# Kernel tuning notes

Hardware: AMD Instinct MI355X
Metric: run time of the kernel (lower is better)

The kernel has to match this reference:

```python
import jax, jax.numpy as jnp
import numpy as np

D = 1024        # inputsize / d_model
G = 8           # groupnum (KV groups)
H = 16          # heads per group
DQ = 128        # qk head dim
DV = 128        # v head dim
FF = 1024       # ffoutsize
B, S = 1, 1024


def _rmsnorm(t, gamma, d_model):
    # torch F.normalize(x, dim=-1) * sqrt(d_model) * gamma
    n = jnp.sqrt(jnp.sum(t * t, axis=-1, keepdims=True))
    return t / jnp.maximum(n, 1e-12) * (d_model ** 0.5) * gamma


def setup_inputs() -> dict:
    key = jax.random.key(0)
    ks = jax.random.split(key, 8)
    std = 0.02
    x = jax.random.normal(ks[0], (B, S, D), dtype=jnp.float32)
    gamma_in = jnp.ones((D,), jnp.float32)
    Wq_w = jax.random.normal(ks[1], (H * G * DQ, D), jnp.float32) * std
    Wq_b = jnp.zeros((H * G * DQ,), jnp.float32)
    Wkv_w = jax.random.normal(ks[2], (G * (DQ + DV), D), jnp.float32) * std
    Wkv_b = jnp.zeros((G * (DQ + DV),), jnp.float32)
    gamma_z = jnp.ones((G * H * DV,), jnp.float32)
    W1 = jax.random.normal(ks[3], (FF * 2, G * H * DV), jnp.float32) * std
    b1 = jnp.zeros((FF * 2,), jnp.float32)
    W2 = jax.random.normal(ks[4], (FF, FF * 2), jnp.float32) * std
    b2 = jnp.zeros((FF,), jnp.float32)
    return {"x": x, "gamma_in": gamma_in, "Wq_w": Wq_w, "Wq_b": Wq_b,
            "Wkv_w": Wkv_w, "Wkv_b": Wkv_b, "gamma_z": gamma_z,
            "W1": W1, "b1": b1, "W2": W2, "b2": b2}


def reference(x, gamma_in, Wq_w, Wq_b, Wkv_w, Wkv_b, gamma_z, W1, b1, W2, b2):
    x = _rmsnorm(x, gamma_in, D)                      # (B,S,D)
    # self-attention path (m is None -> m = x)
    q = (x @ Wq_w.T + Wq_b).reshape(B, S, G, H, DQ)   # (B,S,G,H,dq)
    kv = x @ Wkv_w.T + Wkv_b                          # (B,S,G*(dq+dv))
    k, v = jnp.split(kv, 2, axis=-1)
    k = k.reshape(B, S, G, DQ)                        # (B,S,G,dq)
    v = v.reshape(B, S, G, DV)                        # (B,S,G,dv)
    scale = 1.0 / (DQ ** 0.5)
    scores = jnp.einsum('bsghd,bTgd->bghsT', q, k) * scale  # (B,G,H,S,S)
    attn = jax.nn.softmax(scores, axis=-1)
    z = jnp.einsum('bghsT,bTgd->bsghd', attn, v)      # (B,S,G,H,dv)
    z = z.reshape(B, S, G * H * DV)
    z = _rmsnorm(z, gamma_z, G * H * DV)
    h1 = jax.nn.silu(z @ W1.T + b1)                   # (B,S,2*FF)
    out = jax.nn.silu(h1 @ W2.T + b2)                 # (B,S,FF)
    return out
```

## Files before the change

kernel.cpp:

```cpp
#include <hip/hip_runtime.h>
#include <hip/hip_bf16.h>
#include <math.h>

typedef __attribute__((ext_vector_type(8))) short short8;
typedef __attribute__((ext_vector_type(4))) float floatx4;

__device__ __forceinline__ ushort f2bf(float f) {
  __hip_bfloat16 h = __float2bfloat16(f);
  return *reinterpret_cast<ushort*>(&h);
}
__device__ __forceinline__ float bf2f(ushort u) {
  union { unsigned int i; float f; } c; c.i = ((unsigned)u) << 16; return c.f;
}

__device__ __forceinline__ void lds_dma16(const void* g, void* l) {
  __builtin_amdgcn_global_load_lds((const __attribute__((address_space(1))) void*)g,
                                   (__attribute__((address_space(3))) void*)l, 16, 0, 0);
}

__global__ __launch_bounds__(256) void cvt_all(const float* __restrict__ p0, ushort* __restrict__ o0, int b0,
                                               const float* __restrict__ p1, ushort* __restrict__ o1, int b1,
                                               const float* __restrict__ p2, ushort* __restrict__ o2, int b2,
                                               const float* __restrict__ p3, ushort* __restrict__ o3) {
  int b = blockIdx.x;
  const float* in; ushort* out; int base;
  if (b < b0)            { in = p0; out = o0; base = 0; }
  else if (b < b0 + b1)  { in = p1; out = o1; base = b0; }
  else if (b < b0 + b1 + b2) { in = p2; out = o2; base = b0 + b1; }
  else                   { in = p3; out = o3; base = b0 + b1 + b2; }
  int i = (b - base) * 256 + threadIdx.x;
  float4 v = ((const float4*)in)[i];
  ushort4 o;
  o.x = f2bf(v.x); o.y = f2bf(v.y); o.z = f2bf(v.z); o.w = f2bf(v.w);
  ((ushort4*)out)[i] = o;
}

__global__ __launch_bounds__(256) void rmsnorm_f32(const float* __restrict__ x,
                                                   const float* __restrict__ gamma,
                                                   ushort* __restrict__ y, int D, float sqrtD) {
  const int row = blockIdx.x;
  const float* xr = x + (size_t)row * D;
  float ss = 0.f;
  for (int i = threadIdx.x * 4; i < D; i += 1024) {
    float4 v = *(const float4*)&xr[i];
    ss += v.x * v.x + v.y * v.y + v.z * v.z + v.w * v.w;
  }
#pragma unroll
  for (int off = 1; off < 64; off <<= 1) ss += __shfl_xor(ss, off);
  __shared__ float red[4];
  if ((threadIdx.x & 63) == 0) red[threadIdx.x >> 6] = ss;
  __syncthreads();
  ss = red[0] + red[1] + red[2] + red[3];
  const float sc = sqrtD / fmaxf(sqrtf(ss), 1e-12f);
  for (int i = threadIdx.x * 4; i < D; i += 1024) {
    float4 v = *(const float4*)&xr[i];
    ushort4 o;
    o.x = f2bf(v.x * sc * gamma[i]);
    o.y = f2bf(v.y * sc * gamma[i + 1]);
    o.z = f2bf(v.z * sc * gamma[i + 2]);
    o.w = f2bf(v.w * sc * gamma[i + 3]);
    *(ushort4*)&y[(size_t)row * D + i] = o;
  }
}

__global__ __launch_bounds__(256) void rmsnorm_bf16(const ushort* __restrict__ x,
                                                    const float* __restrict__ gamma,
                                                    ushort* __restrict__ y, int D, float sqrtD) {
  const int row = blockIdx.x;
  const ushort* xr = x + (size_t)row * D;
  float ss = 0.f;
  for (int i = threadIdx.x * 8; i < D; i += 2048) {
    short8 v = *(const short8*)&xr[i];
#pragma unroll
    for (int e = 0; e < 8; e++) { float f = bf2f((ushort)v[e]); ss += f * f; }
  }
#pragma unroll
  for (int off = 1; off < 64; off <<= 1) ss += __shfl_xor(ss, off);
  __shared__ float red[4];
  if ((threadIdx.x & 63) == 0) red[threadIdx.x >> 6] = ss;
  __syncthreads();
  ss = red[0] + red[1] + red[2] + red[3];
  const float sc = sqrtD / fmaxf(sqrtf(ss), 1e-12f);
  for (int i = threadIdx.x * 8; i < D; i += 2048) {
    short8 v = *(const short8*)&xr[i];
    short8 ov;
#pragma unroll
    for (int e = 0; e < 8; e++) ov[e] = (short)f2bf(bf2f((ushort)v[e]) * sc * gamma[i + e]);
    *(short8*)&y[(size_t)row * D + i] = ov;
  }
}

template <int EPI, int ACT, int OUTBF16>
__global__ __launch_bounds__(256, 3) void gemm3(const ushort* __restrict__ A,
                                                const ushort* __restrict__ B,
                                                const float* __restrict__ bias,
                                                const float* __restrict__ bias2,
                                                void* __restrict__ C1,
                                                void* __restrict__ C2,
                                                int M, int N, int K, int Ksplit, float scale) {
  __shared__ ushort As[128 * 64];
  __shared__ ushort Bs[128 * 64];
  const int tid = threadIdx.x;
  const int wave = tid >> 6;
  const int lane = tid & 63;
  const int c16 = lane & 15;
  const int quad = lane >> 4;
  const int wm = wave >> 1;
  const int wn = wave & 1;
  const size_t m0 = (size_t)blockIdx.x * 128;
  const size_t n0 = (size_t)blockIdx.y * 128;
  const int kbeg = blockIdx.z * Ksplit;
  const int kend = kbeg + Ksplit;

  const int rsub = lane >> 3;
  const int csw = (lane & 7) ^ rsub;

  const floatx4 zero = {0.f, 0.f, 0.f, 0.f};
  floatx4 acc[4][4];
#pragma unroll
  for (int a = 0; a < 4; a++)
#pragma unroll
    for (int b = 0; b < 4; b++) acc[a][b] = zero;

  for (int k0 = kbeg; k0 < kend; k0 += 64) {
    __syncthreads();
#pragma unroll
    for (int i = 0; i < 4; i++) {
      const int j = wave * 4 + i;
      const int r = j * 8 + rsub;
      lds_dma16(&A[(m0 + r) * K + k0 + csw * 8], (void*)(As + j * 512));
      lds_dma16(&B[(n0 + r) * K + k0 + csw * 8], (void*)(Bs + j * 512));
    }
    __syncthreads();
#pragma unroll
    for (int kc = 0; kc < 2; kc++) {
      short8 af[4], bf4[4];
#pragma unroll
      for (int mt = 0; mt < 4; mt++) {
        const int row = wm * 64 + mt * 16 + c16;
        af[mt] = *(const short8*)&As[row * 64 + (((kc * 4 + quad) ^ (row & 7)) << 3)];
      }
#pragma unroll
      for (int nt = 0; nt < 4; nt++) {
        const int row = wn * 64 + nt * 16 + c16;
        bf4[nt] = *(const short8*)&Bs[row * 64 + (((kc * 4 + quad) ^ (row & 7)) << 3)];
      }
#pragma unroll
      for (int mt = 0; mt < 4; mt++)
#pragma unroll
        for (int nt = 0; nt < 4; nt++)
          acc[mt][nt] = __builtin_amdgcn_mfma_f32_16x16x32_bf16(af[mt], bf4[nt], acc[mt][nt], 0, 0, 0);
    }
  }

#pragma unroll
  for (int mt = 0; mt < 4; mt++) {
#pragma unroll
    for (int nt = 0; nt < 4; nt++) {
      const size_t col = n0 + wn * 64 + nt * 16 + c16;
      const size_t row0 = m0 + wm * 64 + mt * 16 + quad * 4;
      if (EPI == 0) {
        const float bv = bias[col];
#pragma unroll
        for (int r = 0; r < 4; r++) {
          float v = acc[mt][nt][r] + bv;
          if (ACT) v = v / (1.f + __expf(-v));
          if (OUTBF16) ((ushort*)C1)[(row0 + r) * N + col] = f2bf(v);
          else         ((float*)C1)[(row0 + r) * N + col] = v;
        }
      } else if (EPI == 1) {
        float* plane = (float*)C1 + (size_t)blockIdx.z * M * N;
#pragma unroll
        for (int r = 0; r < 4; r++)
          plane[(row0 + r) * N + col] = acc[mt][nt][r];
      } else {
        if (col < 16384) {
          const float bv = bias[col];
#pragma unroll
          for (int r = 0; r < 4; r++)
            ((ushort*)C1)[(row0 + r) * 16384 + col] = f2bf((acc[mt][nt][r] + bv) * scale);
        } else {
          const size_t ckv = col - 16384;
          const float bv = bias2[ckv];
#pragma unroll
          for (int r = 0; r < 4; r++)
            ((ushort*)C2)[(row0 + r) * 2048 + ckv] = f2bf(acc[mt][nt][r] + bv);
        }
      }
    }
  }
}

template <int NZ, int OUTBF16>
__global__ __launch_bounds__(256) void epi_sum_silu(const float* __restrict__ accb,
                                                    const float* __restrict__ bias,
                                                    void* __restrict__ outp, int N, int n4,
                                                    size_t plane4) {
  int i = blockIdx.x * 256 + threadIdx.x;
  if (i >= n4) return;
  float4 v = ((const float4*)accb)[i];
#pragma unroll
  for (int z = 1; z < NZ; z++) {
    float4 p = ((const float4*)accb)[i + z * plane4];
    v.x += p.x; v.y += p.y; v.z += p.z; v.w += p.w;
  }
  const float4 b = *(const float4*)&bias[(i * 4) % N];
  v.x += b.x; v.y += b.y; v.z += b.z; v.w += b.w;
  v.x = v.x / (1.f + __expf(-v.x));
  v.y = v.y / (1.f + __expf(-v.y));
  v.z = v.z / (1.f + __expf(-v.z));
  v.w = v.w / (1.f + __expf(-v.w));
  if (OUTBF16) {
    ushort4 o; o.x = f2bf(v.x); o.y = f2bf(v.y); o.z = f2bf(v.z); o.w = f2bf(v.w);
    ((ushort4*)outp)[i] = o;
  } else {
    ((float4*)outp)[i] = v;
  }
}

__global__ __launch_bounds__(256) void vtrans(const ushort* __restrict__ KV,
                                              ushort* __restrict__ VT) {
  __shared__ ushort Vl[64 * 138];
  const int tid = threadIdx.x;
  const int t0 = blockIdx.x * 64;
  const int g = blockIdx.y;
#pragma unroll
  for (int i = 0; i < 16; i++) {
    int idx = tid + i * 256;
    int r = idx >> 6, dc = idx & 63;
    *(uint*)&Vl[r * 138 + dc * 2] =
        *(const uint*)&KV[(size_t)(t0 + r) * 2048 + 1024 + g * 128 + dc * 2];
  }
  __syncthreads();
#pragma unroll
  for (int i = 0; i < 4; i++) {
    int idx = tid + i * 256;
    int dv = idx >> 3, tch = idx & 7;
    short8 o;
#pragma unroll
    for (int j = 0; j < 8; j++) o[j] = (short)Vl[(tch * 8 + j) * 138 + dv];
    *(short8*)&VT[(size_t)g * 131072 + (size_t)dv * 1024 + t0 + tch * 8] = o;
  }
}

__global__ __launch_bounds__(512, 2) void attn6(const ushort* __restrict__ Q,
                                                const ushort* __restrict__ KV,
                                                const ushort* __restrict__ VT,
                                                ushort* __restrict__ Z) {
  __shared__ ushort Kl[2][64 * 128];
  __shared__ ushort Vt[2][128 * 64];
  __shared__ ushort Pl[256 * 68];
  __shared__ float  Ls[256];
  const int tid = threadIdx.x;
  const int w = tid >> 6;
  const int lane = tid & 63;
  const int c16 = lane & 15;
  const int quad = lane >> 4;
  const int hh = blockIdx.x >> 2;
  const int qb = blockIdx.x & 3;
  const int g = hh >> 4;
  const int prow0 = (w & 3) * 64;
  const int dv0 = (w >> 2) * 64;

  const ushort* Kg = KV + (size_t)g * 128;
  const ushort* Vg = VT + (size_t)g * 131072;

  short8 aq[2][4];
#pragma unroll
  for (int mt = 0; mt < 2; mt++)
#pragma unroll
    for (int kc = 0; kc < 4; kc++)
      aq[mt][kc] = *(const short8*)&Q[(size_t)(qb * 256 + w * 32 + mt * 16 + c16) * 16384 +
                                      hh * 128 + kc * 32 + quad * 8];

  const floatx4 zero = {0.f, 0.f, 0.f, 0.f};
  floatx4 o[4][4];
  float lacc[2][4];
#pragma unroll
  for (int mt = 0; mt < 4; mt++)
#pragma unroll
    for (int nt = 0; nt < 4; nt++) o[mt][nt] = zero;
#pragma unroll
  for (int mt = 0; mt < 2; mt++)
#pragma unroll
    for (int r = 0; r < 4; r++) lacc[mt][r] = 0.f;

  const int kr16 = lane >> 4;
  const int kc16 = lane & 15;
  const int vr8 = lane >> 3;
  const int vc8 = lane & 7;

  auto stage = [&](int buf, int t0) {
#pragma unroll
    for (int i = 0; i < 2; i++) {
      int krow = w * 8 + i * 4 + kr16;
      int kcs = kc16 ^ (krow & 7);
      lds_dma16(&Kg[(size_t)(t0 + krow) * 2048 + kcs * 8],
                (void*)(&Kl[buf][w * 1024 + i * 512]));
      int vrow = w * 16 + i * 8 + vr8;
      int vcs = vc8 ^ (vrow & 7);
      lds_dma16(&Vg[(size_t)vrow * 1024 + t0 + vcs * 8],
                (void*)(&Vt[buf][w * 1024 + i * 512]));
    }
  };

  stage(0, 0);

  for (int t = 0; t < 16; t++) {
    const int p = t & 1;
    __syncthreads();
    if (t < 15) stage(p ^ 1, (t + 1) * 64);

#pragma unroll
    for (int st = 0; st < 4; st++) {
      floatx4 s0 = zero, s1 = zero;
      const int krow = st * 16 + c16;
#pragma unroll
      for (int kc = 0; kc < 4; kc++) {
        short8 bk = *(const short8*)&Kl[p][krow * 128 + (((kc * 4 + quad) ^ (c16 & 7)) << 3)];
        s0 = __builtin_amdgcn_mfma_f32_16x16x32_bf16(aq[0][kc], bk, s0, 0, 0, 0);
        s1 = __builtin_amdgcn_mfma_f32_16x16x32_bf16(aq[1][kc], bk, s1, 0, 0, 0);
      }
#pragma unroll
      for (int r = 0; r < 4; r++) {
        float p0 = __expf(s0[r]);
        float p1 = __expf(s1[r]);
        lacc[0][r] += p0;
        lacc[1][r] += p1;
        Pl[(w * 32 + quad * 4 + r) * 68 + st * 16 + c16] = f2bf(p0);
        Pl[(w * 32 + 16 + quad * 4 + r) * 68 + st * 16 + c16] = f2bf(p1);
      }
    }
    __syncthreads();

#pragma unroll
    for (int tc = 0; tc < 2; tc++) {
      short8 ap[4];
#pragma unroll
      for (int mt = 0; mt < 4; mt++)
        ap[mt] = *(const short8*)&Pl[(prow0 + mt * 16 + c16) * 68 + tc * 32 + quad * 8];
#pragma unroll
      for (int nt = 0; nt < 4; nt++) {
        const int dv = dv0 + nt * 16 + c16;
        short8 bv = *(const short8*)&Vt[p][dv * 64 + (((tc * 4 + quad) ^ (c16 & 7)) << 3)];
#pragma unroll
        for (int mt = 0; mt < 4; mt++)
          o[mt][nt] = __builtin_amdgcn_mfma_f32_16x16x32_bf16(ap[mt], bv, o[mt][nt], 0, 0, 0);
      }
    }
  }

#pragma unroll
  for (int mt = 0; mt < 2; mt++) {
#pragma unroll
    for (int r = 0; r < 4; r++) {
      float l = lacc[mt][r];
      l += __shfl_xor(l, 1);
      l += __shfl_xor(l, 2);
      l += __shfl_xor(l, 4);
      l += __shfl_xor(l, 8);
      if (c16 == 0) Ls[w * 32 + mt * 16 + quad * 4 + r] = l;
    }
  }
  __syncthreads();

#pragma unroll
  for (int mt = 0; mt < 4; mt++) {
#pragma unroll
    for (int r = 0; r < 4; r++) {
      const float inv = 1.f / Ls[prow0 + mt * 16 + quad * 4 + r];
      const size_t row = (size_t)qb * 256 + prow0 + mt * 16 + quad * 4 + r;
#pragma unroll
      for (int nt = 0; nt < 4; nt++)
        Z[row * 16384 + hh * 128 + dv0 + nt * 16 + c16] = f2bf(o[mt][nt][r] * inv);
    }
  }
}

extern "C" void kernel_launch(void* const* d_in, const int* in_sizes, int n_in,
                              void* d_out, int out_size, void* d_ws, size_t ws_size,
                              hipStream_t stream) {
  (void)in_sizes; (void)n_in; (void)out_size; (void)ws_size;
  const float* x        = (const float*)d_in[0];
  const float* gamma_in = (const float*)d_in[1];
  const float* Wq_w     = (const float*)d_in[2];
  const float* Wq_b     = (const float*)d_in[3];
  const float* Wkv_w    = (const float*)d_in[4];
  const float* Wkv_b    = (const float*)d_in[5];
  const float* gamma_z  = (const float*)d_in[6];
  const float* W1       = (const float*)d_in[7];
  const float* b1       = (const float*)d_in[8];
  const float* W2       = (const float*)d_in[9];
  const float* b2       = (const float*)d_in[10];
  float* out = (float*)d_out;

  char* ws = (char*)d_ws;
  size_t off = 0;
  auto alloc = [&](size_t bytes) {
    void* p = ws + off;
    off += (bytes + 255) & ~(size_t)255;
    return p;
  };
  ushort* xn   = (ushort*)alloc((size_t)1024 * 1024 * 2);
  ushort* Wqb  = (ushort*)alloc((size_t)16384 * 1024 * 2);
  ushort* Wkvb = (ushort*)alloc((size_t)2048 * 1024 * 2);
  ushort* W1b  = (ushort*)alloc((size_t)2048 * 16384 * 2);
  ushort* W2b  = (ushort*)alloc((size_t)1024 * 2048 * 2);
  ushort* Qb   = (ushort*)alloc((size_t)1024 * 16384 * 2);
  ushort* KVb  = (ushort*)alloc((size_t)1024 * 2048 * 2);
  ushort* Zb   = Wqb;
  ushort* VTb  = Wkvb;
  ushort* ZN   = Qb;
  float*  h1f  = (float*)Wqb;
  ushort* H1   = Wkvb;
  float*  outf = (float*)Qb;

  cvt_all<<<16384 + 2048 + 32768 + 2048, 256, 0, stream>>>(
      Wq_w, Wqb, 16384, Wkv_w, Wkvb, 2048, W1, W1b, 32768, W2, W2b);

  rmsnorm_f32<<<1024, 256, 0, stream>>>(x, gamma_in, xn, 1024, 32.0f);

  { dim3 g(8, 144, 1);
    gemm3<2, 0, 1><<<g, 256, 0, stream>>>(xn, Wqb, Wq_b, Wkv_b, Qb, KVb,
                                          1024, 18432, 1024, 1024, 0.08838834764831845f); }

  { dim3 g(16, 8); vtrans<<<g, 256, 0, stream>>>(KVb, VTb); }

  attn6<<<512, 512, 0, stream>>>(Qb, KVb, VTb, Zb);

  rmsnorm_bf16<<<1024, 256, 0, stream>>>(Zb, gamma_z, ZN, 16384, 128.0f);

  { dim3 g(8, 16, 4);
    gemm3<1, 0, 0><<<g, 256, 0, stream>>>(ZN, W1b, b1, nullptr, h1f, nullptr,
                                          1024, 2048, 16384, 4096, 0.f); }
  epi_sum_silu<4, 1><<<2048, 256, 0, stream>>>(h1f, b1, H1, 2048, 1024 * 2048 / 4,
                                               (size_t)1024 * 2048 / 4);

  { dim3 g(8, 8, 4);
    gemm3<1, 0, 0><<<g, 256, 0, stream>>>(H1, W2b, b2, nullptr, outf, nullptr,
                                          1024, 1024, 2048, 512, 0.f); }
  epi_sum_silu<4, 0><<<1024, 256, 0, stream>>>(outf, b2, out, 1024, 1024 * 1024 / 4,
                                               (size_t)1024 * 1024 / 4);
}
```

Before: 580.2 us.

## Shrink attention LDS footprint, swizzle P buffer, remap blocks, add MFMA priority

The attention kernel drops V double-buffering and loads V just-in-time each tile, aliases the row-sum buffer onto the P buffer, and replaces the padded P layout with an XOR-swizzled unpadded one. Together these cut LDS use so that more blocks can reside per CU. Block indices are remapped so neighbouring blocks spread across KV groups, and s_setprio is raised around the MFMA loops. The cost is that the V load is no longer prefetched a tile ahead, so its latency is exposed between the two barriers. An extra barrier is also needed before the aliased Ls is reused.

```diff
diff --git a/kernel.cpp b/kernel.cpp
--- a/kernel.cpp
+++ b/kernel.cpp
@@ -248,16 +248,17 @@
                                                 const ushort* __restrict__ VT,
                                                 ushort* __restrict__ Z) {
   __shared__ ushort Kl[2][64 * 128];
-  __shared__ ushort Vt[2][128 * 64];
-  __shared__ ushort Pl[256 * 68];
-  __shared__ float  Ls[256];
+  __shared__ ushort Vt[128 * 64];
+  __shared__ ushort Pl[256 * 64];
+  float* Ls = (float*)Pl;
   const int tid = threadIdx.x;
   const int w = tid >> 6;
   const int lane = tid & 63;
   const int c16 = lane & 15;
   const int quad = lane >> 4;
-  const int hh = blockIdx.x >> 2;
-  const int qb = blockIdx.x & 3;
+  const int b = (blockIdx.x & 7) * 64 + (blockIdx.x >> 3);
+  const int hh = b >> 2;
+  const int qb = b & 3;
   const int g = hh >> 4;
   const int prow0 = (w & 3) * 64;
   const int dv0 = (w >> 2) * 64;
@@ -290,45 +291,55 @@
   const int vr8 = lane >> 3;
   const int vc8 = lane & 7;
 
-  auto stage = [&](int buf, int t0) {
+  auto stageK = [&](int buf, int t0) {
 #pragma unroll
     for (int i = 0; i < 2; i++) {
       int krow = w * 8 + i * 4 + kr16;
       int kcs = kc16 ^ (krow & 7);
       lds_dma16(&Kg[(size_t)(t0 + krow) * 2048 + kcs * 8],
                 (void*)(&Kl[buf][w * 1024 + i * 512]));
+    }
+  };
+  auto stageV = [&](int t0) {
+#pragma unroll
+    for (int i = 0; i < 2; i++) {
       int vrow = w * 16 + i * 8 + vr8;
       int vcs = vc8 ^ (vrow & 7);
       lds_dma16(&Vg[(size_t)vrow * 1024 + t0 + vcs * 8],
-                (void*)(&Vt[buf][w * 1024 + i * 512]));
+                (void*)(&Vt[w * 1024 + i * 512]));
     }
   };
 
-  stage(0, 0);
+  stageK(0, 0);
 
   for (int t = 0; t < 16; t++) {
     const int p = t & 1;
     __syncthreads();
-    if (t < 15) stage(p ^ 1, (t + 1) * 64);
+    if (t < 15) stageK(p ^ 1, (t + 1) * 64);
+    stageV(t * 64);
 
 #pragma unroll
     for (int st = 0; st < 4; st++) {
       floatx4 s0 = zero, s1 = zero;
       const int krow = st * 16 + c16;
+      __builtin_amdgcn_s_setprio(1);
 #pragma unroll
       for (int kc = 0; kc < 4; kc++) {
         short8 bk = *(const short8*)&Kl[p][krow * 128 + (((kc * 4 + quad) ^ (c16 & 7)) << 3)];
         s0 = __builtin_amdgcn_mfma_f32_16x16x32_bf16(aq[0][kc], bk, s0, 0, 0, 0);
         s1 = __builtin_amdgcn_mfma_f32_16x16x32_bf16(aq[1][kc], bk, s1, 0, 0, 0);
       }
+      __builtin_amdgcn_s_setprio(0);
 #pragma unroll
       for (int r = 0; r < 4; r++) {
         float p0 = __expf(s0[r]);
         float p1 = __expf(s1[r]);
         lacc[0][r] += p0;
         lacc[1][r] += p1;
-        Pl[(w * 32 + quad * 4 + r) * 68 + st * 16 + c16] = f2bf(p0);
-        Pl[(w * 32 + 16 + quad * 4 + r) * 68 + st * 16 + c16] = f2bf(p1);
+        const int rlo = w * 32 + quad * 4 + r;
+        const int sw = ((((st * 2) + (c16 >> 3)) ^ (rlo & 7)) << 3) | (c16 & 7);
+        Pl[rlo * 64 + sw] = f2bf(p0);
+        Pl[(rlo + 16) * 64 + sw] = f2bf(p1);
       }
     }
     __syncthreads();
@@ -337,19 +348,24 @@
     for (int tc = 0; tc < 2; tc++) {
       short8 ap[4];
 #pragma unroll
-      for (int mt = 0; mt < 4; mt++)
-        ap[mt] = *(const short8*)&Pl[(prow0 + mt * 16 + c16) * 68 + tc * 32 + quad * 8];
+      for (int mt = 0; mt < 4; mt++) {
+        const int row = prow0 + mt * 16 + c16;
+        ap[mt] = *(const short8*)&Pl[row * 64 + (((tc * 4 + quad) ^ (c16 & 7)) << 3)];
+      }
+      __builtin_amdgcn_s_setprio(1);
 #pragma unroll
       for (int nt = 0; nt < 4; nt++) {
         const int dv = dv0 + nt * 16 + c16;
-        short8 bv = *(const short8*)&Vt[p][dv * 64 + (((tc * 4 + quad) ^ (c16 & 7)) << 3)];
+        short8 bv = *(const short8*)&Vt[dv * 64 + (((tc * 4 + quad) ^ (c16 & 7)) << 3)];
 #pragma unroll
         for (int mt = 0; mt < 4; mt++)
           o[mt][nt] = __builtin_amdgcn_mfma_f32_16x16x32_bf16(ap[mt], bv, o[mt][nt], 0, 0, 0);
       }
-    }
-  }
-
+      __builtin_amdgcn_s_setprio(0);
+    }
+  }
+
+  __syncthreads();
 #pragma unroll
   for (int mt = 0; mt < 2; mt++) {
 #pragma unroll
```

New measurement: 575.4 us. About the same (-0.8%).
